# Kernel optimization log

Measured on AMD Instinct MI355X. Metric: run time of the kernel, lower is better.

## Reference

```python
import jax, jax.numpy as jnp
import numpy as np

N, C, K = 300000, 64, 27  # active voxels, channels, 3^3 kernel offsets


def sparse_conv(x, nbr, mask, W, b):
    """MinkowskiConvolution as gather -> GEMM -> accumulate.
    x: [N, C] features; nbr: [N, K] int32 neighbor index per kernel offset;
    mask: [N, K] bool validity; W: [K, C, C]; b: [C].
    out[i] = b + sum_k mask[i,k] * x[nbr[i,k]] @ W[k]
    Scans over the K=27 fixed kernel offsets so only an [N, C] gathered
    buffer is live at a time (never materializes [N, K, C]).
    """
    def step(acc, kin):
        Wk, nk, mk = kin
        g = jnp.where(mk[:, None], x[nk], jnp.zeros((), x.dtype))  # [N, C] gather
        return acc + g @ Wk, None

    acc0 = jnp.zeros_like(x) + b
    out, _ = jax.lax.scan(step, acc0, (W, nbr.T, mask.T))
    return out


def setup_inputs() -> dict:
    key = jax.random.key(0)
    ks = jax.random.split(key, 7)
    features = jax.random.normal(ks[0], (N, C), dtype=jnp.float32)
    neighbor_idx = jax.random.randint(ks[1], (N, K), 0, N, dtype=jnp.int32)
    neighbor_mask = jax.random.uniform(ks[2], (N, K)) < 0.6  # variable neighbor counts
    scale = 1.0 / np.sqrt(K * C)
    W0 = jax.random.normal(ks[3], (K, C, C), dtype=jnp.float32) * scale
    b0 = jax.random.normal(ks[4], (C,), dtype=jnp.float32) * 0.01
    W1 = jax.random.normal(ks[5], (K, C, C), dtype=jnp.float32) * scale
    b1 = jax.random.normal(ks[6], (C,), dtype=jnp.float32) * 0.01
    return {
        "features": features,
        "neighbor_idx": neighbor_idx,
        "neighbor_mask": neighbor_mask,
        "W0": W0, "b0": b0, "W1": W1, "b1": b1,
    }


def reference(features, neighbor_idx, neighbor_mask, W0, b0, W1, b1):
    # conv0 -> ReLU -> conv1 -> residual add (stride=1, shared kernel map)
    out = sparse_conv(features, neighbor_idx, neighbor_mask, W0, b0)
    out = jax.nn.relu(out)
    out = sparse_conv(out, neighbor_idx, neighbor_mask, W1, b1)
    return out + features
```

## Files before the change

### kernel.cpp

```cpp
#include <hip/hip_runtime.h>
#include <hip/hip_bf16.h>
#include <stdint.h>

typedef __bf16 bf16x8 __attribute__((ext_vector_type(8)));
typedef float f32x4 __attribute__((ext_vector_type(4)));
typedef unsigned short u16x4 __attribute__((ext_vector_type(4)));

__device__ __forceinline__ unsigned short f2bf(float f) {
    union { float f; uint32_t u; } v; v.f = f;
    uint32_t u = v.u;
    return (unsigned short)((u + 0x7fffu + ((u >> 16) & 1u)) >> 16);
}

__global__ __launch_bounds__(256) void prep_x(const f32x4* __restrict__ x,
                                              u16x4* __restrict__ xb, int n4, int n4tot) {
    int t = blockIdx.x * 256 + threadIdx.x;
    if (t < n4) {
        f32x4 v = x[t];
        u16x4 o;
        o.x = f2bf(v.x); o.y = f2bf(v.y); o.z = f2bf(v.z); o.w = f2bf(v.w);
        xb[t] = o;
    } else if (t < n4tot) {
        u16x4 z = {0, 0, 0, 0};
        xb[t] = z;
    }
}

__global__ void zero_row(unsigned short* __restrict__ p, long off) {
    p[off + threadIdx.x] = 0;
}

__global__ __launch_bounds__(256) void prep_w(const float* __restrict__ W,
                                              unsigned short* __restrict__ Wt, int K) {
    int k = blockIdx.x;
    unsigned short* Wtk = Wt + (size_t)k * 4608;
    const float* Wk = W + (size_t)k * 4096;
    for (int j = threadIdx.x; j < 4608; j += 256) {
        int co = j / 72, ci = j % 72;
        unsigned short v = 0;
        if (k < K && ci < 64) v = f2bf(Wk[ci * 64 + co]);
        Wtk[j] = v;
    }
}

__global__ void detect_mask(const unsigned int* __restrict__ m, int* __restrict__ flag) {
    __shared__ int s_not_int, s_not_f32;
    if (threadIdx.x == 0) { s_not_int = 0; s_not_f32 = 0; }
    __syncthreads();
    unsigned int w = m[threadIdx.x];
    if (w > 1u) s_not_int = 1;
    if (w != 0u && w != 0x3f800000u) s_not_f32 = 1;
    __syncthreads();
    if (threadIdx.x == 0) *flag = s_not_int ? (s_not_f32 ? 1 : 2) : 0;
}

template <int IOFF>
__device__ __forceinline__ bf16x8 gl16(const unsigned short* base, unsigned voff) {
    bf16x8 r;
    asm volatile("global_load_dwordx4 %0, %1, %2 offset:%c3"
                 : "=v"(r) : "v"(voff), "s"(base), "i"(IOFF));
    return r;
}

struct Slot { bf16x8 f[8]; };

template <int NW>
__device__ __forceinline__ void waitv(Slot& s) {
    asm volatile("s_waitcnt vmcnt(%c8)"
                 : "+v"(s.f[0]), "+v"(s.f[1]), "+v"(s.f[2]), "+v"(s.f[3]),
                   "+v"(s.f[4]), "+v"(s.f[5]), "+v"(s.f[6]), "+v"(s.f[7])
                 : "i"(NW));
    __builtin_amdgcn_sched_barrier(0);
}

__device__ __forceinline__ void gload_lds16(const unsigned short* g, unsigned short* l) {
    __builtin_amdgcn_global_load_lds(
        (const __attribute__((address_space(1))) void*)(const void*)g,
        (__attribute__((address_space(3))) void*)(void*)l, 16, 0, 0);
}

template <int MODE>
__global__ __launch_bounds__(256, 2) void conv_mfma(
    const unsigned short* __restrict__ xb,
    const int* __restrict__ nbr,
    const void* __restrict__ maskp,
    const int* __restrict__ flagp,
    const unsigned short* __restrict__ Wt,
    const float* __restrict__ bias,
    const float* __restrict__ resid,
    void* __restrict__ outp,
    int N, int K)
{
    __shared__ unsigned short Wlds[2][18432];

    const int tid = threadIdx.x;
    const int wv  = tid >> 6;
    const int l   = tid & 63;
    const int lr  = l & 15;
    const int lg  = l >> 4;
    const int wavebase = blockIdx.x * 256 + wv * 64;

    const int myrow = wavebase + l;
    const int mr = myrow < N ? myrow : N - 1;

    unsigned mbits = 0;
    {
        const int flag = *flagp;
        long moff = (long)mr * K;
        if (flag == 1) {
            const unsigned char* mp = (const unsigned char*)maskp + moff;
#pragma unroll
            for (int k = 0; k < 27; ++k) mbits |= (mp[k] ? 1u : 0u) << k;
        } else if (flag == 0) {
            const int* mp = (const int*)maskp + moff;
#pragma unroll
            for (int k = 0; k < 27; ++k) mbits |= (mp[k] ? 1u : 0u) << k;
        } else {
            const float* mp = (const float*)maskp + moff;
#pragma unroll
            for (int k = 0; k < 27; ++k) mbits |= ((mp[k] != 0.f) ? 1u : 0u) << k;
        }
    }

    unsigned o[28];
    {
        const int* nrow = nbr + (long)mr * K;
#pragma unroll
        for (int k = 0; k < 27; ++k) {
            unsigned g = ((mbits >> k) & 1u) ? (unsigned)nrow[k] : (unsigned)N;
            o[k] = g * 128u;
        }
        o[27] = (unsigned)N * 128u;
    }

    const int bpa0 = (0 * 16 + lr) * 4;
    const int bpa1 = (1 * 16 + lr) * 4;
    const int bpa2 = (2 * 16 + lr) * 4;
    const int bpa3 = (3 * 16 + lr) * 4;
    const unsigned chk = (unsigned)(lg << 4);

    const int lrw = lr * 72 + lg * 8;

    f32x4 acc[4][4] = {};
    Slot pipe[2];
    bf16x8 Bf[8];

#define STAGE(P) do { \
    const unsigned short* _src = Wt + (size_t)(P) * 18432 + wv * 4608 + (l << 3); \
    unsigned short* _dst = &Wlds[(P) & 1][wv * 4608]; \
    _Pragma("unroll") \
    for (int _s = 0; _s < 9; ++_s) \
        gload_lds16(_src + _s * 512, _dst + _s * 512); \
    asm volatile("" ::: "memory"); \
} while (0)

#define GISSUE(J) do { \
    unsigned _b0 = (unsigned)__builtin_amdgcn_ds_bpermute(bpa0, (int)o[J]) + chk; \
    unsigned _b1 = (unsigned)__builtin_amdgcn_ds_bpermute(bpa1, (int)o[J]) + chk; \
    unsigned _b2 = (unsigned)__builtin_amdgcn_ds_bpermute(bpa2, (int)o[J]) + chk; \
    unsigned _b3 = (unsigned)__builtin_amdgcn_ds_bpermute(bpa3, (int)o[J]) + chk; \
    Slot& _s = pipe[(J) & 1]; \
    _s.f[0] = gl16<0 >(xb, _b0); _s.f[1] = gl16<64>(xb, _b0); \
    _s.f[2] = gl16<0 >(xb, _b1); _s.f[3] = gl16<64>(xb, _b1); \
    _s.f[4] = gl16<0 >(xb, _b2); _s.f[5] = gl16<64>(xb, _b2); \
    _s.f[6] = gl16<0 >(xb, _b3); _s.f[7] = gl16<64>(xb, _b3); \
} while (0)

#define BLOAD(J) do { \
    const unsigned short* _wl = &Wlds[((J) >> 2) & 1][((J) & 3) * 4608]; \
    _Pragma("unroll") \
    for (int ct = 0; ct < 4; ++ct) { \
        const unsigned short* _wp = _wl + ct * 1152 + lrw; \
        Bf[ct * 2]     = *(const bf16x8*)(_wp); \
        Bf[ct * 2 + 1] = *(const bf16x8*)(_wp + 32); \
    } \
} while (0)

#define MFMA16(J) do { \
    Slot& _s = pipe[(J) & 1]; \
    _Pragma("unroll") \
    for (int ct = 0; ct < 4; ++ct) { \
        _Pragma("unroll") \
        for (int at = 0; at < 4; ++at) { \
            acc[at][ct] = __builtin_amdgcn_mfma_f32_16x16x32_bf16(_s.f[at * 2],     Bf[ct * 2],     acc[at][ct], 0, 0, 0); \
            acc[at][ct] = __builtin_amdgcn_mfma_f32_16x16x32_bf16(_s.f[at * 2 + 1], Bf[ct * 2 + 1], acc[at][ct], 0, 0, 0); \
        } \
    } \
} while (0)

#define FENCE() do { \
    asm volatile("s_waitcnt vmcnt(16)" ::: "memory"); \
    __builtin_amdgcn_sched_barrier(0); \
    __builtin_amdgcn_s_barrier(); \
    __builtin_amdgcn_sched_barrier(0); \
} while (0)

#define STEP(J, NW) do { BLOAD(J); waitv<NW>(pipe[(J) & 1]); MFMA16(J); } while (0)

    STAGE(0);
    GISSUE(0); GISSUE(1);
    asm volatile("s_waitcnt vmcnt(16)" ::: "memory");
    __builtin_amdgcn_sched_barrier(0);
    __builtin_amdgcn_s_barrier();
    __builtin_amdgcn_sched_barrier(0);

    STAGE(1); STEP(0, 17); GISSUE(2);
    STEP(1, 17); GISSUE(3);
    STEP(2, 8);  GISSUE(4);
    STEP(3, 8);  GISSUE(5);
    FENCE();
    STAGE(2); STEP(4, 17); GISSUE(6);
    STEP(5, 17); GISSUE(7);
    STEP(6, 8);  GISSUE(8);
    STEP(7, 8);  GISSUE(9);
    FENCE();
    STAGE(3); STEP(8, 17); GISSUE(10);
    STEP(9, 17);  GISSUE(11);
    STEP(10, 8);  GISSUE(12);
    STEP(11, 8);  GISSUE(13);
    FENCE();
    STAGE(4); STEP(12, 17); GISSUE(14);
    STEP(13, 17); GISSUE(15);
    STEP(14, 8);  GISSUE(16);
    STEP(15, 8);  GISSUE(17);
    FENCE();
    STAGE(5); STEP(16, 17); GISSUE(18);
    STEP(17, 17); GISSUE(19);
    STEP(18, 8);  GISSUE(20);
    STEP(19, 8);  GISSUE(21);
    FENCE();
    STAGE(6); STEP(20, 17); GISSUE(22);
    STEP(21, 17); GISSUE(23);
    STEP(22, 8);  GISSUE(24);
    STEP(23, 8);  GISSUE(25);
    FENCE();
    STEP(24, 8);  GISSUE(26);
    STEP(25, 8);  GISSUE(27);
    STEP(26, 8);
    STEP(27, 0);

#pragma unroll
    for (int at = 0; at < 4; ++at) {
#pragma unroll
        for (int ct = 0; ct < 4; ++ct) {
            int col = ct * 16 + lr;
            float bv = bias[col];
#pragma unroll
            for (int rg = 0; rg < 4; ++rg) {
                int row = wavebase + at * 16 + lg * 4 + rg;
                if (row < N) {
                    long oo = (long)row * 64 + col;
                    float v = acc[at][ct][rg] + bv;
                    if (MODE == 0) {
                        ((unsigned short*)outp)[oo] = f2bf(v > 0.f ? v : 0.f);
                    } else {
                        ((float*)outp)[oo] = v + resid[oo];
                    }
                }
            }
        }
    }

#undef STAGE
#undef GISSUE
#undef BLOAD
#undef MFMA16
#undef FENCE
#undef STEP
}

static inline size_t align256(size_t x) { return (x + 255) & ~(size_t)255; }

extern "C" void kernel_launch(void* const* d_in, const int* in_sizes, int n_in,
                              void* d_out, int out_size, void* d_ws, size_t ws_size,
                              hipStream_t stream) {
    const float* x    = (const float*)d_in[0];
    const int*   nbr  = (const int*)d_in[1];
    const void*  mask = d_in[2];
    const float* W0   = (const float*)d_in[3];
    const float* b0   = (const float*)d_in[4];
    const float* W1   = (const float*)d_in[5];
    const float* b1   = (const float*)d_in[6];

    const int NC = in_sizes[0];
    const int N  = NC / 64;
    const int K  = in_sizes[1] / N;
    const int KP = 28;

    char* ws = (char*)d_ws;
    size_t xb_bytes = (size_t)(NC + 64) * 2;
    size_t wt_bytes = (size_t)KP * 4608 * 2;
    size_t xb_off   = 0;
    size_t hb_off   = xb_off + align256(xb_bytes);
    size_t wt0_off  = hb_off + align256(xb_bytes);
    size_t wt1_off  = wt0_off + align256(wt_bytes);
    size_t flag_off = wt1_off + align256(wt_bytes);

    unsigned short* xb  = (unsigned short*)(ws + xb_off);
    unsigned short* hb  = (unsigned short*)(ws + hb_off);
    unsigned short* wt0 = (unsigned short*)(ws + wt0_off);
    unsigned short* wt1 = (unsigned short*)(ws + wt1_off);
    int* flag           = (int*)(ws + flag_off);

    int n4 = NC / 4;
    int n4tot = n4 + 16;
    prep_x<<<(n4tot + 255) / 256, 256, 0, stream>>>((const f32x4*)x, (u16x4*)xb, n4, n4tot);
    zero_row<<<1, 64, 0, stream>>>(hb, (long)NC);
    prep_w<<<KP, 256, 0, stream>>>(W0, wt0, K);
    prep_w<<<KP, 256, 0, stream>>>(W1, wt1, K);
    detect_mask<<<1, 1024, 0, stream>>>((const unsigned int*)mask, flag);

    int nblocks = (N + 255) / 256;
    conv_mfma<0><<<nblocks, 256, 0, stream>>>(xb, nbr, mask, flag, wt0, b0, nullptr, hb, N, K);
    conv_mfma<1><<<nblocks, 256, 0, stream>>>(hb, nbr, mask, flag, wt1, b1, x, d_out, N, K);
}
```

Measured before the change: 357.3 us.

## Prepack weights in MFMA fragment order and read bf16 residual

Weights are prepacked per kernel offset in the exact per-lane MFMA B-fragment order. This removes the 72-stride padded layout, so each B load is a contiguous 16-byte read per lane. LDS staging shrinks to two offsets per buffer half, giving a 32KB footprint and a 13-phase pipeline with more barriers. The residual add now reads the bf16 copy of the input instead of fp32, which halves that traffic but adds rounding error to the output.

```diff
diff --git a/kernel.cpp b/kernel.cpp
--- a/kernel.cpp
+++ b/kernel.cpp
@@ -10,6 +10,11 @@
     union { float f; uint32_t u; } v; v.f = f;
     uint32_t u = v.u;
     return (unsigned short)((u + 0x7fffu + ((u >> 16) & 1u)) >> 16);
+}
+
+__device__ __forceinline__ float bf2f(unsigned short b) {
+    union { uint32_t u; float f; } v; v.u = ((uint32_t)b) << 16;
+    return v.f;
 }
 
 __global__ __launch_bounds__(256) void prep_x(const f32x4* __restrict__ x,
@@ -31,15 +36,18 @@
 }
 
 __global__ __launch_bounds__(256) void prep_w(const float* __restrict__ W,
-                                              unsigned short* __restrict__ Wt, int K) {
+                                              unsigned short* __restrict__ Wf, int K) {
     int k = blockIdx.x;
-    unsigned short* Wtk = Wt + (size_t)k * 4608;
+    unsigned short* Wfk = Wf + (size_t)k * 4096;
     const float* Wk = W + (size_t)k * 4096;
-    for (int j = threadIdx.x; j < 4608; j += 256) {
-        int co = j / 72, ci = j % 72;
-        unsigned short v = 0;
-        if (k < K && ci < 64) v = f2bf(Wk[ci * 64 + co]);
-        Wtk[j] = v;
+    for (int idx = threadIdx.x; idx < 4096; idx += 256) {
+        int j   = idx & 7;
+        int l   = (idx >> 3) & 63;
+        int c2h = idx >> 9;
+        int ct  = c2h >> 1, h = c2h & 1;
+        int ci  = h * 32 + (l >> 4) * 8 + j;
+        int co  = ct * 16 + (l & 15);
+        Wfk[idx] = (k < K) ? f2bf(Wk[ci * 64 + co]) : (unsigned short)0;
     }
 }
 
@@ -85,13 +93,13 @@
     const int* __restrict__ nbr,
     const void* __restrict__ maskp,
     const int* __restrict__ flagp,
-    const unsigned short* __restrict__ Wt,
+    const unsigned short* __restrict__ Wf,
     const float* __restrict__ bias,
-    const float* __restrict__ resid,
+    const unsigned short* __restrict__ residb,
     void* __restrict__ outp,
     int N, int K)
 {
-    __shared__ unsigned short Wlds[2][18432];
+    __shared__ unsigned short Wlds[16384];
 
     const int tid = threadIdx.x;
     const int wv  = tid >> 6;
@@ -139,17 +147,15 @@
     const int bpa3 = (3 * 16 + lr) * 4;
     const unsigned chk = (unsigned)(lg << 4);
 
-    const int lrw = lr * 72 + lg * 8;
-
     f32x4 acc[4][4] = {};
     Slot pipe[2];
     bf16x8 Bf[8];
 
 #define STAGE(P) do { \
-    const unsigned short* _src = Wt + (size_t)(P) * 18432 + wv * 4608 + (l << 3); \
-    unsigned short* _dst = &Wlds[(P) & 1][wv * 4608]; \
+    const unsigned short* _src = Wf + (size_t)(P) * 8192 + wv * 2048 + (l << 3); \
+    unsigned short* _dst = &Wlds[((P) & 1) * 8192 + wv * 2048]; \
     _Pragma("unroll") \
-    for (int _s = 0; _s < 9; ++_s) \
+    for (int _s = 0; _s < 4; ++_s) \
         gload_lds16(_src + _s * 512, _dst + _s * 512); \
     asm volatile("" ::: "memory"); \
 } while (0)
@@ -167,13 +173,10 @@
 } while (0)
 
 #define BLOAD(J) do { \
-    const unsigned short* _wl = &Wlds[((J) >> 2) & 1][((J) & 3) * 4608]; \
+    const unsigned short* _wl = &Wlds[(((J) >> 1) & 1) * 8192 + ((J) & 1) * 4096]; \
     _Pragma("unroll") \
-    for (int ct = 0; ct < 4; ++ct) { \
-        const unsigned short* _wp = _wl + ct * 1152 + lrw; \
-        Bf[ct * 2]     = *(const bf16x8*)(_wp); \
-        Bf[ct * 2 + 1] = *(const bf16x8*)(_wp + 32); \
-    } \
+    for (int _c = 0; _c < 8; ++_c) \
+        Bf[_c] = *(const bf16x8*)(_wl + _c * 512 + l * 8); \
 } while (0)
 
 #define MFMA16(J) do { \
@@ -197,6 +200,13 @@
 
 #define STEP(J, NW) do { BLOAD(J); waitv<NW>(pipe[(J) & 1]); MFMA16(J); } while (0)
 
+#define PHASE(PH1, K0) do { \
+    STAGE(PH1); \
+    STEP(K0, 12);       GISSUE((K0) + 2); \
+    STEP((K0) + 1, 12); GISSUE((K0) + 3); \
+    FENCE(); \
+} while (0)
+
     STAGE(0);
     GISSUE(0); GISSUE(1);
     asm volatile("s_waitcnt vmcnt(16)" ::: "memory");
@@ -204,38 +214,10 @@
     __builtin_amdgcn_s_barrier();
     __builtin_amdgcn_sched_barrier(0);
 
-    STAGE(1); STEP(0, 17); GISSUE(2);
-    STEP(1, 17); GISSUE(3);
-    STEP(2, 8);  GISSUE(4);
-    STEP(3, 8);  GISSUE(5);
-    FENCE();
-    STAGE(2); STEP(4, 17); GISSUE(6);
-    STEP(5, 17); GISSUE(7);
-    STEP(6, 8);  GISSUE(8);
-    STEP(7, 8);  GISSUE(9);
-    FENCE();
-    STAGE(3); STEP(8, 17); GISSUE(10);
-    STEP(9, 17);  GISSUE(11);
-    STEP(10, 8);  GISSUE(12);
-    STEP(11, 8);  GISSUE(13);
-    FENCE();
-    STAGE(4); STEP(12, 17); GISSUE(14);
-    STEP(13, 17); GISSUE(15);
-    STEP(14, 8);  GISSUE(16);
-    STEP(15, 8);  GISSUE(17);
-    FENCE();
-    STAGE(5); STEP(16, 17); GISSUE(18);
-    STEP(17, 17); GISSUE(19);
-    STEP(18, 8);  GISSUE(20);
-    STEP(19, 8);  GISSUE(21);
-    FENCE();
-    STAGE(6); STEP(20, 17); GISSUE(22);
-    STEP(21, 17); GISSUE(23);
-    STEP(22, 8);  GISSUE(24);
-    STEP(23, 8);  GISSUE(25);
-    FENCE();
-    STEP(24, 8);  GISSUE(26);
-    STEP(25, 8);  GISSUE(27);
+    PHASE(1, 0);   PHASE(2, 2);   PHASE(3, 4);   PHASE(4, 6);
+    PHASE(5, 8);   PHASE(6, 10);  PHASE(7, 12);  PHASE(8, 14);
+    PHASE(9, 16);  PHASE(10, 18); PHASE(11, 20); PHASE(12, 22);
+    PHASE(13, 24);
     STEP(26, 8);
     STEP(27, 0);
 
@@ -254,7 +236,7 @@
                     if (MODE == 0) {
                         ((unsigned short*)outp)[oo] = f2bf(v > 0.f ? v : 0.f);
                     } else {
-                        ((float*)outp)[oo] = v + resid[oo];
+                        ((float*)outp)[oo] = v + bf2f(residb[oo]);
                     }
                 }
             }
@@ -267,6 +249,7 @@
 #undef MFMA16
 #undef FENCE
 #undef STEP
+#undef PHASE
 }
 
 static inline size_t align256(size_t x) { return (x + 255) & ~(size_t)255; }
@@ -289,7 +272,7 @@
 
     char* ws = (char*)d_ws;
     size_t xb_bytes = (size_t)(NC + 64) * 2;
-    size_t wt_bytes = (size_t)KP * 4608 * 2;
+    size_t wt_bytes = (size_t)KP * 4096 * 2;
     size_t xb_off   = 0;
     size_t hb_off   = xb_off + align256(xb_bytes);
     size_t wt0_off  = hb_off + align256(xb_bytes);
@@ -298,19 +281,19 @@
 
     unsigned short* xb  = (unsigned short*)(ws + xb_off);
     unsigned short* hb  = (unsigned short*)(ws + hb_off);
-    unsigned short* wt0 = (unsigned short*)(ws + wt0_off);
-    unsigned short* wt1 = (unsigned short*)(ws + wt1_off);
+    unsigned short* wf0 = (unsigned short*)(ws + wt0_off);
+    unsigned short* wf1 = (unsigned short*)(ws + wt1_off);
     int* flag           = (int*)(ws + flag_off);
 
     int n4 = NC / 4;
     int n4tot = n4 + 16;
     prep_x<<<(n4tot + 255) / 256, 256, 0, stream>>>((const f32x4*)x, (u16x4*)xb, n4, n4tot);
     zero_row<<<1, 64, 0, stream>>>(hb, (long)NC);
-    prep_w<<<KP, 256, 0, stream>>>(W0, wt0, K);
-    prep_w<<<KP, 256, 0, stream>>>(W1, wt1, K);
+    prep_w<<<KP, 256, 0, stream>>>(W0, wf0, K);
+    prep_w<<<KP, 256, 0, stream>>>(W1, wf1, K);
     detect_mask<<<1, 1024, 0, stream>>>((const unsigned int*)mask, flag);
 
     int nblocks = (N + 255) / 256;
-    conv_mfma<0><<<nblocks, 256, 0, stream>>>(xb, nbr, mask, flag, wt0, b0, nullptr, hb, N, K);
-    conv_mfma<1><<<nblocks, 256, 0, stream>>>(hb, nbr, mask, flag, wt1, b1, x, d_out, N, K);
-}
+    conv_mfma<0><<<nblocks, 256, 0, stream>>>(xb, nbr, mask, flag, wf0, b0, nullptr, hb, N, K);
+    conv_mfma<1><<<nblocks, 256, 0, stream>>>(hb, nbr, mask, flag, wf1, b1, xb, d_out, N, K);
+}
```

New measurement: 339.4 us. 5.0% less time.
